# Performance work log

Measured on AMD Instinct MI355X. Metric: run time of the kernel, lower is better.

Reference implementation:

```python
import jax, jax.numpy as jnp
import numpy as np
from jax import lax

B, P = 32, 1024          # batch, max_phonemes
V, E, H = 100, 512, 512  # vocab, embedding_dim, hidden_dim
EPS = 1e-5


def setup_inputs() -> dict:
    key = jax.random.key(0)
    ks = jax.random.split(key, 12)
    return {
        "phoneme_ids": jax.random.randint(ks[0], (B, P), 0, V),
        "phoneme_durations": jax.random.randint(ks[1], (B, P), 0, 10),
        "emb": jax.random.normal(ks[2], (V, E), jnp.float32) * 0.02,
        "conv1_w": jax.random.normal(ks[3], (H, E, 3), jnp.float32) * 0.02,
        "conv1_b": jnp.zeros((H,), jnp.float32),
        "bn1_gamma": 1.0 + 0.1 * jax.random.normal(ks[4], (H,), jnp.float32),
        "bn1_beta": 0.1 * jax.random.normal(ks[5], (H,), jnp.float32),
        "bn1_mean": jnp.zeros((H,), jnp.float32),
        "bn1_var": jnp.ones((H,), jnp.float32),
        "conv2_w": jax.random.normal(ks[6], (H, H, 3), jnp.float32) * 0.02,
        "conv2_b": jnp.zeros((H,), jnp.float32),
        "bn2_gamma": 1.0 + 0.1 * jax.random.normal(ks[7], (H,), jnp.float32),
        "bn2_beta": 0.1 * jax.random.normal(ks[8], (H,), jnp.float32),
        "bn2_mean": jnp.zeros((H,), jnp.float32),
        "bn2_var": jnp.ones((H,), jnp.float32),
    }


def _conv_bn_relu(x, w, b, gamma, beta, mean, var):
    # x: [B, C, P]; w: [O, C, 3]; 'same' padding conv1d, inference batchnorm, relu
    y = lax.conv_general_dilated(x, w, (1,), [(1, 1)],
                                 dimension_numbers=("NCH", "OIH", "NCH"))
    y = y + b[None, :, None]
    scale = gamma * lax.rsqrt(var + EPS)
    y = y * scale[None, :, None] + (beta - mean * scale)[None, :, None]
    return jax.nn.relu(y)


def _upsample(x, durations):
    # x: [B, H, P], durations: [B, P] int -> [B, H, max_frames]
    cum = jnp.cumsum(durations, axis=1)              # [B, P]
    total = cum[:, -1]                               # [B]
    max_frames = int(jnp.max(total))                 # concrete (data-derived shape)
    frames = jnp.arange(max_frames)                  # [F]
    # frame f belongs to phoneme p iff cum[p-1] <= f < cum[p]
    idx = jax.vmap(lambda c: jnp.searchsorted(c, frames, side="right"))(cum)
    idx = jnp.minimum(idx, P - 1)                    # [B, F]
    gathered = jnp.take_along_axis(x, idx[:, None, :], axis=2)  # [B, H, F]
    mask = (frames[None, :] < total[:, None]).astype(x.dtype)   # [B, F]
    return gathered * mask[:, None, :]


def reference(phoneme_ids, phoneme_durations, emb,
              conv1_w, conv1_b, bn1_gamma, bn1_beta, bn1_mean, bn1_var,
              conv2_w, conv2_b, bn2_gamma, bn2_beta, bn2_mean, bn2_var):
    x = emb[phoneme_ids]                 # [B, P, E]
    x = jnp.transpose(x, (0, 2, 1))      # [B, E, P]
    x = _conv_bn_relu(x, conv1_w, conv1_b, bn1_gamma, bn1_beta, bn1_mean, bn1_var)
    x = _conv_bn_relu(x, conv2_w, conv2_b, bn2_gamma, bn2_beta, bn2_mean, bn2_var)
    return _upsample(x, phoneme_durations)
```

## Files before the change

kernel.cpp:

```cpp
#include <hip/hip_runtime.h>

#define B_ 32
#define P_ 1024
#define V_ 100
#define E_ 512
#define H_ 512
#define C_ 512
#define EPS_ 1e-5f

typedef float f32x4 __attribute__((ext_vector_type(4)));
typedef short bf16x8 __attribute__((ext_vector_type(8)));

#define GLB(p) ((const __attribute__((address_space(1))) unsigned int*)(p))
#define LDSP(p) ((__attribute__((address_space(3))) unsigned int*)(p))

__device__ __forceinline__ unsigned short f2bf(float f) {
  unsigned int u = __float_as_uint(f);
  u += 0x7fffu + ((u >> 16) & 1u);
  return (unsigned short)(u >> 16);
}
__device__ __forceinline__ float bf2f(unsigned short s) {
  return __uint_as_float(((unsigned int)s) << 16);
}

__global__ __launch_bounds__(256) void w1t_kernel(const float* __restrict__ w1,
                                                  float* __restrict__ w1T) {
  __shared__ float tile[64][65];
  int h0 = blockIdx.x * 64;
  int e0 = blockIdx.y * 64;
  int t = threadIdx.x;
  int c = t & 63, r4 = t >> 6;
#pragma unroll
  for (int r = 0; r < 64; r += 4)
    tile[r + r4][c] = w1[(size_t)(h0 + r + r4) * 1536 + e0 + c];
  __syncthreads();
#pragma unroll
  for (int r = 0; r < 64; r += 4)
    w1T[(size_t)(e0 + r + r4) * 512 + h0 + c] = tile[c][r + r4];
}

__global__ __launch_bounds__(64) void g_kernel(const float* __restrict__ emb,
                                               const float* __restrict__ w1T,
                                               const float* __restrict__ g1,
                                               const float* __restrict__ vr1,
                                               float* __restrict__ G) {
  __shared__ float se[E_];
  int v = blockIdx.x;
  int h = blockIdx.y * 64 + threadIdx.x;
  for (int i = threadIdx.x; i < E_; i += 64) se[i] = emb[(size_t)v * E_ + i];
  __syncthreads();
  float a0 = 0.f, a1 = 0.f, a2 = 0.f;
#pragma unroll 4
  for (int e = 0; e < E_; ++e) {
    float x = se[e];
    const float* wp = w1T + (size_t)(3 * e) * H_ + h;
    a0 = fmaf(wp[0], x, a0);
    a1 = fmaf(wp[H_], x, a1);
    a2 = fmaf(wp[2 * H_], x, a2);
  }
  float sc = g1[h] * rsqrtf(vr1[h] + EPS_);
  G[((size_t)0 * V_ + v) * H_ + h] = a0 * sc;
  G[((size_t)1 * V_ + v) * H_ + h] = a1 * sc;
  G[((size_t)2 * V_ + v) * H_ + h] = a2 * sc;
}

__global__ __launch_bounds__(256) void a2_kernel(
    const float* __restrict__ w2, const float* __restrict__ b1,
    const float* __restrict__ g1, const float* __restrict__ be1,
    const float* __restrict__ mn1, const float* __restrict__ vr1,
    const float* __restrict__ b2, const float* __restrict__ g2,
    const float* __restrict__ be2, const float* __restrict__ mn2,
    const float* __restrict__ vr2, float* __restrict__ bias1,
    float* __restrict__ bias2, unsigned short* __restrict__ A2h,
    unsigned short* __restrict__ A2l) {
  int h = blockIdx.x;
  int tid = threadIdx.x;
  float sc1 = g1[h] * rsqrtf(vr1[h] + EPS_);
  float sc2 = g2[h] * rsqrtf(vr2[h] + EPS_);
  if (tid == 0) {
    bias1[h] = b1[h] * sc1 + be1[h] - mn1[h] * sc1;
    bias2[h] = b2[h] * sc2 + be2[h] - mn2[h] * sc2;
  }
  for (int j = tid; j < 3 * C_; j += 256) {
    int k = j >> 9;
    int c = j & (C_ - 1);
    float val = w2[((size_t)h * C_ + c) * 3 + k] * sc2;
    unsigned short hi = f2bf(val);
    A2h[(size_t)h * (3 * C_) + j] = hi;
    A2l[(size_t)h * (3 * C_) + j] = f2bf(val - bf2f(hi));
  }
}

__global__ __launch_bounds__(256) void embed_conv1_kernel(
    const int* __restrict__ ids, const float* __restrict__ G,
    const float* __restrict__ bias1, unsigned short* __restrict__ Bh,
    unsigned short* __restrict__ Bl) {
  int r = blockIdx.x % (P_ + 2);
  int b = blockIdx.x / (P_ + 2);
  int t = threadIdx.x;
  size_t outbase = ((size_t)b * (P_ + 2) + r) * C_;
  unsigned int* BhU = (unsigned int*)(Bh + outbase);
  unsigned int* BlU = (unsigned int*)(Bl + outbase);
  if (r == 0 || r == P_ + 1) {
    BhU[t] = 0u;
    BlU[t] = 0u;
    return;
  }
  int p = r - 1;
  int v0 = (p >= 1) ? ids[b * P_ + p - 1] : -1;
  int v1 = ids[b * P_ + p];
  int v2 = (p + 1 < P_) ? ids[b * P_ + p + 1] : -1;
  const float2* G0 = (v0 >= 0) ? (const float2*)(G + ((size_t)0 * V_ + v0) * H_) : nullptr;
  const float2* G1 = (const float2*)(G + ((size_t)1 * V_ + v1) * H_);
  const float2* G2 = (v2 >= 0) ? (const float2*)(G + ((size_t)2 * V_ + v2) * H_) : nullptr;
  const float2* bi = (const float2*)bias1;

  float2 s = bi[t];
  float2 gm = G1[t];
  s.x += gm.x;
  s.y += gm.y;
  if (G0) { float2 g0 = G0[t]; s.x += g0.x; s.y += g0.y; }
  if (G2) { float2 g2v = G2[t]; s.x += g2v.x; s.y += g2v.y; }
  s.x = fmaxf(s.x, 0.f);
  s.y = fmaxf(s.y, 0.f);
  unsigned short h0 = f2bf(s.x), h1 = f2bf(s.y);
  unsigned short l0 = f2bf(s.x - bf2f(h0)), l1 = f2bf(s.y - bf2f(h1));
  BhU[t] = (unsigned int)h0 | ((unsigned int)h1 << 16);
  BlU[t] = (unsigned int)l0 | ((unsigned int)l1 << 16);
}

__global__ __launch_bounds__(1024) void cumsum_kernel(const int* __restrict__ dur,
                                                      int* __restrict__ cum) {
  __shared__ int s[P_];
  int b = blockIdx.x;
  int t = threadIdx.x;
  s[t] = dur[b * P_ + t];
  __syncthreads();
  for (int off = 1; off < P_; off <<= 1) {
    int v = (t >= off) ? s[t - off] : 0;
    __syncthreads();
    s[t] += v;
    __syncthreads();
  }
  cum[b * P_ + t] = s[t];
}

struct BTrue  { static constexpr bool v = true;  };
struct BFalse { static constexpr bool v = false; };

__global__ __launch_bounds__(512, 2) void conv2_gemm8_kernel(
    const unsigned short* __restrict__ A2h, const unsigned short* __restrict__ A2l,
    const unsigned short* __restrict__ Bh, const unsigned short* __restrict__ Bl,
    const float* __restrict__ bias2, unsigned short* __restrict__ out2b) {
  __shared__ __align__(16) unsigned short sm[4][16384];

  const int tid = threadIdx.x;
  const int wid = tid >> 6;
  const int lane = tid & 63;
  const int wm = wid >> 2, wn = wid & 3;
  const int fr = lane & 15, fq = lane >> 4;

  int bid = blockIdx.x;
  int wg = (bid & 7) * 32 + (bid >> 3);
  int m0 = (wg & 1) * 256;
  int n0 = (wg >> 1) * 256;
  int bb = n0 >> 10;
  int p0 = n0 & (P_ - 1);

  const unsigned short* Arow_h = A2h + (size_t)m0 * 1536;
  const unsigned short* Arow_l = A2l + (size_t)m0 * 1536;
  const size_t boff = ((size_t)bb * (P_ + 2) + p0) * 512;
  const unsigned short* Brow_h = Bh + boff;
  const unsigned short* Brow_l = Bl + boff;

  const int srow = tid >> 3;
  const int scol = (((tid & 7) ^ ((tid >> 3) & 7))) * 8;
  const int ldsw = wid * 512;

  auto stageA = [&](int kt, int blk) {
    const unsigned short* base = (kt < 48) ? Arow_h : Arow_l;
    int kl = (kt % 24) * 64;
    const unsigned short* src = base + (size_t)(blk * 64 + srow) * 1536 + kl + scol;
    __builtin_amdgcn_global_load_lds(GLB(src), LDSP(&sm[kt & 1][blk * 4096 + ldsw]), 16, 0, 0);
  };
  auto stageB = [&](int kt, int blk) {
    const unsigned short* base = (kt >= 24 && kt < 48) ? Brow_l : Brow_h;
    int kl = (kt % 24) * 64;
    const unsigned short* src = base + (size_t)(blk * 64 + srow) * 512 + kl + scol;
    __builtin_amdgcn_global_load_lds(GLB(src), LDSP(&sm[2 + (kt & 1)][blk * 4096 + ldsw]), 16, 0, 0);
  };

  f32x4 acc[8][4] = {};

  const int rA0 = wm * 128 + fr;
  const int rB0 = wn * 64 + fr;
  const int cxor = fr & 7;

  auto rdA = [&](bf16x8 (&af)[4][2], int buf, int mh) {
#pragma unroll
    for (int m = 0; m < 4; ++m)
#pragma unroll
      for (int ks = 0; ks < 2; ++ks)
        af[m][ks] = *(const bf16x8*)&sm[buf][(rA0 + mh * 64 + m * 16) * 64 +
                                            ((ks * 4 + fq) ^ cxor) * 8];
  };
  auto rdB = [&](bf16x8 (&bv)[2][2], int buf, int nh) {
#pragma unroll
    for (int n = 0; n < 2; ++n)
#pragma unroll
      for (int ks = 0; ks < 2; ++ks)
        bv[n][ks] = *(const bf16x8*)&sm[2 + buf][(rB0 + nh * 32 + n * 16) * 64 +
                                                 ((ks * 4 + fq) ^ cxor) * 8];
  };

#define SYNC_HEAD()                                      \
  __builtin_amdgcn_sched_barrier(0);                     \
  __builtin_amdgcn_s_barrier();                          \
  asm volatile("s_waitcnt lgkmcnt(0)" ::: "memory");     \
  __builtin_amdgcn_sched_barrier(0);                     \
  __builtin_amdgcn_s_setprio(1)

#define SYNC_TAIL()                                      \
  __builtin_amdgcn_s_setprio(0);                         \
  __builtin_amdgcn_sched_barrier(0);                     \
  __builtin_amdgcn_s_barrier();                          \
  __builtin_amdgcn_sched_barrier(0)

#define MFMA_QUAD(mh, nh, AF, BF)                                              \
  _Pragma("unroll") for (int m = 0; m < 4; ++m)                                \
  _Pragma("unroll") for (int n = 0; n < 2; ++n)                                \
  _Pragma("unroll") for (int ks = 0; ks < 2; ++ks)                             \
    acc[(mh) * 4 + m][(nh) * 2 + n] = __builtin_amdgcn_mfma_f32_16x16x32_bf16( \
        AF[m][ks], BF[n][ks], acc[(mh) * 4 + m][(nh) * 2 + n], 0, 0, 0)

#pragma unroll
  for (int blk = 0; blk < 4; ++blk) { stageA(0, blk); stageB(0, blk); }
  stageA(1, 0); stageA(1, 2);
  asm volatile("s_waitcnt vmcnt(2)" ::: "memory");
  __builtin_amdgcn_sched_barrier(0);
  __builtin_amdgcn_s_barrier();
  __builtin_amdgcn_sched_barrier(0);

  int kt = 0;
  auto iter = [&](auto lasttag) {
    constexpr bool LAST = decltype(lasttag)::v;
    bf16x8 af[4][2], bv[2][2];
    rdA(af, 0, 0); rdB(bv, 0, 0);
    stageA(kt + 1, 1); stageA(kt + 1, 3); stageB(kt + 1, 0);
    SYNC_HEAD(); MFMA_QUAD(0, 0, af, bv); SYNC_TAIL();

    rdB(bv, 0, 1);
    stageB(kt + 1, 1); stageB(kt + 1, 2); stageB(kt + 1, 3);
    SYNC_HEAD(); MFMA_QUAD(0, 1, af, bv); SYNC_TAIL();

    rdA(af, 0, 1); rdB(bv, 0, 0);
    if constexpr (!LAST) { stageA(kt + 2, 0); stageA(kt + 2, 2); }
    SYNC_HEAD(); MFMA_QUAD(1, 0, af, bv); SYNC_TAIL();

    rdB(bv, 0, 1);
    __builtin_amdgcn_sched_barrier(0);
    __builtin_amdgcn_s_barrier();
    asm volatile("s_waitcnt lgkmcnt(0)" ::: "memory");
    __builtin_amdgcn_sched_barrier(0);
    __builtin_amdgcn_s_setprio(1);
    MFMA_QUAD(1, 1, af, bv);
    __builtin_amdgcn_s_setprio(0);
    __builtin_amdgcn_sched_barrier(0);
    if constexpr (LAST) asm volatile("s_waitcnt vmcnt(0)" ::: "memory");
    else                asm volatile("s_waitcnt vmcnt(2)" ::: "memory");
    __builtin_amdgcn_s_barrier();
    __builtin_amdgcn_sched_barrier(0);

    rdA(af, 1, 0); rdB(bv, 1, 0);
    if constexpr (!LAST) { stageA(kt + 2, 1); stageA(kt + 2, 3); stageB(kt + 2, 0); }
    SYNC_HEAD(); MFMA_QUAD(0, 0, af, bv); SYNC_TAIL();

    rdB(bv, 1, 1);
    if constexpr (!LAST) { stageB(kt + 2, 1); stageB(kt + 2, 2); stageB(kt + 2, 3); }
    SYNC_HEAD(); MFMA_QUAD(0, 1, af, bv); SYNC_TAIL();

    rdA(af, 1, 1); rdB(bv, 1, 0);
    if constexpr (!LAST) { stageA(kt + 3, 0); stageA(kt + 3, 2); }
    SYNC_HEAD(); MFMA_QUAD(1, 0, af, bv); SYNC_TAIL();

    rdB(bv, 1, 1);
    __builtin_amdgcn_sched_barrier(0);
    __builtin_amdgcn_s_barrier();
    asm volatile("s_waitcnt lgkmcnt(0)" ::: "memory");
    __builtin_amdgcn_sched_barrier(0);
    __builtin_amdgcn_s_setprio(1);
    MFMA_QUAD(1, 1, af, bv);
    __builtin_amdgcn_s_setprio(0);
    __builtin_amdgcn_sched_barrier(0);
    if constexpr (!LAST) {
      asm volatile("s_waitcnt vmcnt(2)" ::: "memory");
      __builtin_amdgcn_s_barrier();
      __builtin_amdgcn_sched_barrier(0);
    }
    kt += 2;
  };

  for (int i = 0; i < 35; ++i) iter(BFalse{});
  iter(BTrue{});

#pragma unroll
  for (int ai = 0; ai < 8; ++ai) {
    int row = m0 + wm * 128 + (ai >> 2) * 64 + (ai & 3) * 16 + fq * 4;
#pragma unroll
    for (int bj = 0; bj < 4; ++bj) {
      int col = n0 + wn * 64 + (bj >> 1) * 32 + (bj & 1) * 16 + fr;
      int bb2 = col >> 10;
      int p = col & (P_ - 1);
#pragma unroll
      for (int r = 0; r < 4; ++r) {
        float v = acc[ai][bj][r] + bias2[row + r];
        out2b[((size_t)bb2 * H_ + row + r) * P_ + p] = f2bf(fmaxf(v, 0.f));
      }
    }
  }
#undef SYNC_HEAD
#undef SYNC_TAIL
#undef MFMA_QUAD
}

__global__ __launch_bounds__(256) void upsample_kernel(const unsigned short* __restrict__ out2b,
                                                       const int* __restrict__ cum,
                                                       float* __restrict__ out, int T) {
  __shared__ int sc[P_];
  int b = blockIdx.z;
  int h0 = blockIdx.y * 64;
  int tid = threadIdx.x;
  for (int i = tid; i < P_; i += 256) sc[i] = cum[b * P_ + i];
  __syncthreads();
  int t = blockIdx.x * 256 + tid;
  if (t >= T) return;
  int tot = sc[P_ - 1];
  bool valid = (t < tot);
  int lo = 0, hi = P_;
  while (lo < hi) {
    int mid = (lo + hi) >> 1;
    if (sc[mid] <= t) lo = mid + 1; else hi = mid;
  }
  int idx = min(lo, P_ - 1);
  const unsigned short* src = out2b + ((size_t)b * H_ + h0) * P_ + idx;
  float* dst = out + ((size_t)b * H_ + h0) * T + t;
  if (valid) {
#pragma unroll 8
    for (int h = 0; h < 64; ++h) dst[(size_t)h * T] = bf2f(src[(size_t)h * P_]);
  } else {
#pragma unroll 8
    for (int h = 0; h < 64; ++h) dst[(size_t)h * T] = 0.f;
  }
}

static inline size_t align256(size_t x) { return (x + 255) & ~(size_t)255; }

extern "C" void kernel_launch(void* const* d_in, const int* in_sizes, int n_in,
                              void* d_out, int out_size, void* d_ws, size_t ws_size,
                              hipStream_t stream) {
  const int*   ids = (const int*)d_in[0];
  const int*   dur = (const int*)d_in[1];
  const float* emb = (const float*)d_in[2];
  const float* w1  = (const float*)d_in[3];
  const float* b1  = (const float*)d_in[4];
  const float* g1  = (const float*)d_in[5];
  const float* be1 = (const float*)d_in[6];
  const float* mn1 = (const float*)d_in[7];
  const float* vr1 = (const float*)d_in[8];
  const float* w2  = (const float*)d_in[9];
  const float* b2  = (const float*)d_in[10];
  const float* g2  = (const float*)d_in[11];
  const float* be2 = (const float*)d_in[12];
  const float* mn2 = (const float*)d_in[13];
  const float* vr2 = (const float*)d_in[14];
  float* out = (float*)d_out;

  int T = out_size / (B_ * H_);

  char* ws = (char*)d_ws;
  size_t off = 0;
  auto carve = [&](size_t bytes) { void* p = ws + off; off = align256(off + bytes); return p; };
  float* G              = (float*)carve((size_t)3 * V_ * H_ * 4);
  float* w1T            = (float*)carve((size_t)3 * E_ * H_ * 4);
  float* bias1          = (float*)carve(H_ * 4);
  float* bias2          = (float*)carve(H_ * 4);
  unsigned short* A2h   = (unsigned short*)carve((size_t)H_ * 3 * C_ * 2);
  unsigned short* A2l   = (unsigned short*)carve((size_t)H_ * 3 * C_ * 2);
  unsigned short* Bhv   = (unsigned short*)carve((size_t)B_ * (P_ + 2) * C_ * 2);
  unsigned short* Blv   = (unsigned short*)carve((size_t)B_ * (P_ + 2) * C_ * 2);
  unsigned short* out2b = (unsigned short*)carve((size_t)B_ * H_ * P_ * 2);
  int* cum              = (int*)carve((size_t)B_ * P_ * 4);

  w1t_kernel<<<dim3(H_ / 64, (3 * E_) / 64), 256, 0, stream>>>(w1, w1T);
  a2_kernel<<<H_, 256, 0, stream>>>(w2, b1, g1, be1, mn1, vr1, b2, g2, be2, mn2, vr2,
                                    bias1, bias2, A2h, A2l);
  g_kernel<<<dim3(V_, H_ / 64), 64, 0, stream>>>(emb, w1T, g1, vr1, G);
  embed_conv1_kernel<<<B_ * (P_ + 2), 256, 0, stream>>>(ids, G, bias1, Bhv, Blv);
  cumsum_kernel<<<B_, P_, 0, stream>>>(dur, cum);
  conv2_gemm8_kernel<<<256, 512, 0, stream>>>(A2h, A2l, Bhv, Blv, bias2, out2b);
  upsample_kernel<<<dim3((T + 255) / 256, H_ / 64, B_), 256, 0, stream>>>(out2b, cum, out, T);
}
```

Baseline: 619.8 us.

## Store conv2 output as [B,P,H] and vectorize upsample writes along time

The conv2 epilogue now writes its bf16 output transposed to [B, P, H], packing four consecutive hidden rows into one 8-byte store. The upsample kernel first computes per-frame phoneme indices into shared memory. Each thread then owns one hidden channel and writes four consecutive frames per float4 store, with gathers running along H so that neighbouring lanes read contiguous memory. This targets uncoalesced strided gathers and scalar output stores. The cost is a shared-memory staging step and a separate scalar path for partial tiles.

```diff
diff --git a/kernel.cpp b/kernel.cpp
--- a/kernel.cpp
+++ b/kernel.cpp
@@ -151,7 +151,7 @@
 __global__ __launch_bounds__(512, 2) void conv2_gemm8_kernel(
     const unsigned short* __restrict__ A2h, const unsigned short* __restrict__ A2l,
     const unsigned short* __restrict__ Bh, const unsigned short* __restrict__ Bl,
-    const float* __restrict__ bias2, unsigned short* __restrict__ out2b) {
+    const float* __restrict__ bias2, unsigned short* __restrict__ out2T) {
   __shared__ __align__(16) unsigned short sm[4][16384];
 
   const int tid = threadIdx.x;
@@ -311,11 +311,14 @@
       int col = n0 + wn * 64 + (bj >> 1) * 32 + (bj & 1) * 16 + fr;
       int bb2 = col >> 10;
       int p = col & (P_ - 1);
-#pragma unroll
-      for (int r = 0; r < 4; ++r) {
-        float v = acc[ai][bj][r] + bias2[row + r];
-        out2b[((size_t)bb2 * H_ + row + r) * P_ + p] = f2bf(fmaxf(v, 0.f));
-      }
+      float v0 = fmaxf(acc[ai][bj][0] + bias2[row + 0], 0.f);
+      float v1 = fmaxf(acc[ai][bj][1] + bias2[row + 1], 0.f);
+      float v2 = fmaxf(acc[ai][bj][2] + bias2[row + 2], 0.f);
+      float v3 = fmaxf(acc[ai][bj][3] + bias2[row + 3], 0.f);
+      uint2 pk;
+      pk.x = (unsigned int)f2bf(v0) | ((unsigned int)f2bf(v1) << 16);
+      pk.y = (unsigned int)f2bf(v2) | ((unsigned int)f2bf(v3) << 16);
+      *(uint2*)&out2T[((size_t)bb2 * P_ + p) * H_ + row] = pk;
     }
   }
 #undef SYNC_HEAD
@@ -323,33 +326,58 @@
 #undef MFMA_QUAD
 }
 
-__global__ __launch_bounds__(256) void upsample_kernel(const unsigned short* __restrict__ out2b,
+__global__ __launch_bounds__(256) void upsample_kernel(const unsigned short* __restrict__ out2T,
                                                        const int* __restrict__ cum,
                                                        float* __restrict__ out, int T) {
   __shared__ int sc[P_];
+  __shared__ int idx_sh[256];
   int b = blockIdx.z;
   int h0 = blockIdx.y * 64;
   int tid = threadIdx.x;
   for (int i = tid; i < P_; i += 256) sc[i] = cum[b * P_ + i];
   __syncthreads();
-  int t = blockIdx.x * 256 + tid;
-  if (t >= T) return;
+  int t0 = blockIdx.x * 256;
   int tot = sc[P_ - 1];
-  bool valid = (t < tot);
-  int lo = 0, hi = P_;
-  while (lo < hi) {
-    int mid = (lo + hi) >> 1;
-    if (sc[mid] <= t) lo = mid + 1; else hi = mid;
-  }
-  int idx = min(lo, P_ - 1);
-  const unsigned short* src = out2b + ((size_t)b * H_ + h0) * P_ + idx;
-  float* dst = out + ((size_t)b * H_ + h0) * T + t;
-  if (valid) {
-#pragma unroll 8
-    for (int h = 0; h < 64; ++h) dst[(size_t)h * T] = bf2f(src[(size_t)h * P_]);
+  {
+    int t = t0 + tid;
+    int lo = 0, hi = P_;
+    while (lo < hi) {
+      int mid = (lo + hi) >> 1;
+      if (sc[mid] <= t) lo = mid + 1; else hi = mid;
+    }
+    idx_sh[tid] = (t < tot) ? min(lo, P_ - 1) : -1;
+  }
+  __syncthreads();
+  int h = tid & 63;
+  int g = tid >> 6;
+  const unsigned short* src = out2T + (size_t)b * P_ * H_ + h0 + h;
+  float* dst = out + (size_t)(b * H_ + h0 + h) * T;
+  bool full = (t0 + 256 <= T) && ((T & 3) == 0);
+  if (full) {
+    for (int pass = 0; pass < 16; ++pass) {
+      int tq = (pass * 4 + g) * 4;
+      float4 o;
+      int e0 = idx_sh[tq + 0], e1 = idx_sh[tq + 1];
+      int e2 = idx_sh[tq + 2], e3 = idx_sh[tq + 3];
+      o.x = (e0 >= 0) ? bf2f(src[(size_t)e0 * H_]) : 0.f;
+      o.y = (e1 >= 0) ? bf2f(src[(size_t)e1 * H_]) : 0.f;
+      o.z = (e2 >= 0) ? bf2f(src[(size_t)e2 * H_]) : 0.f;
+      o.w = (e3 >= 0) ? bf2f(src[(size_t)e3 * H_]) : 0.f;
+      *(float4*)&dst[t0 + tq] = o;
+    }
   } else {
-#pragma unroll 8
-    for (int h = 0; h < 64; ++h) dst[(size_t)h * T] = 0.f;
+    for (int pass = 0; pass < 16; ++pass) {
+      int tq = (pass * 4 + g) * 4;
+#pragma unroll
+      for (int u = 0; u < 4; ++u) {
+        int q = tq + u;
+        int t = t0 + q;
+        if (t < T) {
+          int e = idx_sh[q];
+          dst[t] = (e >= 0) ? bf2f(src[(size_t)e * H_]) : 0.f;
+        }
+      }
+    }
   }
 }
 
@@ -388,7 +416,7 @@
   unsigned short* A2l   = (unsigned short*)carve((size_t)H_ * 3 * C_ * 2);
   unsigned short* Bhv   = (unsigned short*)carve((size_t)B_ * (P_ + 2) * C_ * 2);
   unsigned short* Blv   = (unsigned short*)carve((size_t)B_ * (P_ + 2) * C_ * 2);
-  unsigned short* out2b = (unsigned short*)carve((size_t)B_ * H_ * P_ * 2);
+  unsigned short* out2T = (unsigned short*)carve((size_t)B_ * P_ * H_ * 2);
   int* cum              = (int*)carve((size_t)B_ * P_ * 4);
 
   w1t_kernel<<<dim3(H_ / 64, (3 * E_) / 64), 256, 0, stream>>>(w1, w1T);
@@ -397,6 +425,6 @@
   g_kernel<<<dim3(V_, H_ / 64), 64, 0, stream>>>(emb, w1T, g1, vr1, G);
   embed_conv1_kernel<<<B_ * (P_ + 2), 256, 0, stream>>>(ids, G, bias1, Bhv, Blv);
   cumsum_kernel<<<B_, P_, 0, stream>>>(dur, cum);
-  conv2_gemm8_kernel<<<256, 512, 0, stream>>>(A2h, A2l, Bhv, Blv, bias2, out2b);
-  upsample_kernel<<<dim3((T + 255) / 256, H_ / 64, B_), 256, 0, stream>>>(out2b, cum, out, T);
-}
+  conv2_gemm8_kernel<<<256, 512, 0, stream>>>(A2h, A2l, Bhv, Blv, bias2, out2T);
+  upsample_kernel<<<dim3((T + 255) / 256, H_ / 64, B_), 256, 0, stream>>>(out2T, cum, out, T);
+}
```

Result: slower. 961.5 us (+55.1%).
